# Kernel optimization log

Measured on AMD Instinct MI355X. Metric: run time of the kernel, lower is better.

Reference implementation:

```python
import jax, jax.numpy as jnp
import numpy as np

V, E, B, C = 10000, 128, 16, 128
N_REL = 8

def setup_inputs() -> dict:
    key = jax.random.key(0)
    k1, k2, k3, k4, k5 = jax.random.split(key, 5)
    src = jax.random.randint(k1, (B, C), 0, V, dtype=jnp.int32)
    src_embed = jax.random.normal(k2, (B, C, E), dtype=jnp.float32)
    embed_weight = jax.random.normal(k3, (V, E), dtype=jnp.float32)
    edge_matrix = jax.random.uniform(k4, (V, V), dtype=jnp.float32)
    relation_matrix = jax.random.randint(k5, (V, V), 0, 9, dtype=jnp.int32)
    return {"src": src, "src_embed": src_embed, "embed_weight": embed_weight,
            "edge_matrix": edge_matrix, "relation_matrix": relation_matrix}

def reference(src, src_embed, embed_weight, edge_matrix, relation_matrix):
    # base scores against full vocab: [B, C, V]
    base = jnp.einsum('bce,ve->bcv', src_embed, embed_weight)
    # gather the rows of both tables once: [B, C, V]
    edge_rows = edge_matrix[src]
    rel_rows = relation_matrix[src]
    concept_embeddings = []
    scores = []
    for i in range(N_REL):
        # ((relation_matrix == i+1) * edge_matrix)[src] > 0, gathered form
        mask = (jnp.where(rel_rows == i + 1, edge_rows, 0.0) > 0).astype(base.dtype)
        concept_weights = mask * base                     # [B, C, V]
        attn = jax.nn.softmax(concept_weights, axis=2)     # softmax over full vocab
        ce = jnp.einsum('bcv,ve->bce', attn, embed_weight) # [B, C, E]
        concept_embeddings.append(ce)
        scores.append(jnp.sum(src_embed * ce, axis=2, keepdims=True))
    scores = jnp.concatenate(scores, axis=2)               # [B, C, 8]
    weights = jax.nn.softmax(scores, axis=2)
    final = jnp.zeros_like(src_embed)
    for i in range(N_REL):
        final = final + weights[:, :, i:i + 1] * concept_embeddings[i]
    return final
```

## Files before the change

### kernel.cpp

```cpp
#include <hip/hip_runtime.h>

#define VV 10000
#define EE 128
#define NROWS 2048
#define NSPLIT 16

__global__ __launch_bounds__(256) void k1_base_gemm(
    const float* __restrict__ SE,
    const float* __restrict__ W,
    float* __restrict__ base)
{
    __shared__ float As[32 * 132];
    __shared__ float Ws[32 * 132];
    const int tid = threadIdx.x;
    const int v0 = blockIdx.x * 128;
    const int n0 = blockIdx.y * 128;
    const int tx = tid & 15;
    const int ty = tid >> 4;

    float acc[8][8];
    #pragma unroll
    for (int i = 0; i < 8; i++)
        #pragma unroll
        for (int j = 0; j < 8; j++) acc[i][j] = 0.f;

    for (int e0 = 0; e0 < EE; e0 += 32) {
        #pragma unroll
        for (int p = 0; p < 4; p++) {
            int f = tid + p * 256;
            int row = f >> 3;
            int c4  = f & 7;
            float4 a = *(const float4*)(SE + (n0 + row) * EE + e0 + c4 * 4);
            As[(c4 * 4 + 0) * 132 + row] = a.x;
            As[(c4 * 4 + 1) * 132 + row] = a.y;
            As[(c4 * 4 + 2) * 132 + row] = a.z;
            As[(c4 * 4 + 3) * 132 + row] = a.w;
            int vrow = v0 + row;
            float4 b = (vrow < VV) ? *(const float4*)(W + vrow * EE + e0 + c4 * 4)
                                   : make_float4(0.f, 0.f, 0.f, 0.f);
            Ws[(c4 * 4 + 0) * 132 + row] = b.x;
            Ws[(c4 * 4 + 1) * 132 + row] = b.y;
            Ws[(c4 * 4 + 2) * 132 + row] = b.z;
            Ws[(c4 * 4 + 3) * 132 + row] = b.w;
        }
        __syncthreads();
        #pragma unroll 4
        for (int kk = 0; kk < 32; kk++) {
            float4 a0 = *(const float4*)(As + kk * 132 + ty * 8);
            float4 a1 = *(const float4*)(As + kk * 132 + ty * 8 + 4);
            float4 b0 = *(const float4*)(Ws + kk * 132 + tx * 8);
            float4 b1 = *(const float4*)(Ws + kk * 132 + tx * 8 + 4);
            float av[8] = {a0.x, a0.y, a0.z, a0.w, a1.x, a1.y, a1.z, a1.w};
            float bv[8] = {b0.x, b0.y, b0.z, b0.w, b1.x, b1.y, b1.z, b1.w};
            #pragma unroll
            for (int i = 0; i < 8; i++)
                #pragma unroll
                for (int j = 0; j < 8; j++)
                    acc[i][j] = fmaf(av[i], bv[j], acc[i][j]);
        }
        __syncthreads();
    }

    #pragma unroll
    for (int i = 0; i < 8; i++) {
        int n = n0 + ty * 8 + i;
        float* brow = base + (long long)n * VV;
        #pragma unroll
        for (int jj = 0; jj < 2; jj++) {
            int v = v0 + tx * 8 + jj * 4;
            if (v < VV)
                *(float4*)(brow + v) = make_float4(acc[i][jj * 4 + 0], acc[i][jj * 4 + 1],
                                                   acc[i][jj * 4 + 2], acc[i][jj * 4 + 3]);
        }
    }
}

__global__ __launch_bounds__(256) void k2_stats(
    const int*   __restrict__ src,
    const float* __restrict__ edge,
    const int*   __restrict__ rel,
    float* __restrict__ baseA)
{
    __shared__ float seb[VV];
    __shared__ unsigned char srb[VV];
    __shared__ float wred[33][4];
    __shared__ float fin[33];
    __shared__ float cvals[12];

    const int n = blockIdx.x;
    const int tid = threadIdx.x;
    const int lane = tid & 63;
    const int wv = tid >> 6;
    const int s = src[n];
    const float4* brow4 = (const float4*)(baseA + (long long)n * VV);
    const float4* erow4 = (const float4*)(edge + (long long)s * VV);
    const int4*   rrow4 = (const int4*)(rel + (long long)s * VV);

    float accv[33];
    #pragma unroll
    for (int i = 0; i < 33; i++) accv[i] = 0.f;

    for (int v4 = tid; v4 < VV / 4; v4 += 256) {
        float4 b = brow4[v4];
        float4 e = erow4[v4];
        int4   r = rrow4[v4];
        float bb[4] = {b.x, b.y, b.z, b.w};
        float ee[4] = {e.x, e.y, e.z, e.w};
        int   rr[4] = {r.x, r.y, r.z, r.w};
        #pragma unroll
        for (int c = 0; c < 4; c++) {
            int rb = (rr[c] >= 1 && rr[c] <= 8 && ee[c] > 0.f) ? rr[c] : 0;
            float bc = bb[c];
            float eb = __expf(bc);
            float beb = bc * eb;
            seb[v4 * 4 + c] = eb;
            srb[v4 * 4 + c] = (unsigned char)rb;
            accv[0] += bc;
            #pragma unroll
            for (int q = 0; q < 8; q++) {
                float m = (rb == q + 1) ? 1.f : 0.f;
                accv[1 + q]  += m;
                accv[9 + q]  = fmaf(m, bc,  accv[9 + q]);
                accv[17 + q] = fmaf(m, eb,  accv[17 + q]);
                accv[25 + q] = fmaf(m, beb, accv[25 + q]);
            }
        }
    }

    #pragma unroll
    for (int i = 0; i < 33; i++) {
        float x = accv[i];
        #pragma unroll
        for (int off = 32; off > 0; off >>= 1) x += __shfl_xor(x, off, 64);
        if (lane == 0) wred[i][wv] = x;
    }
    __syncthreads();
    if (tid < 33)
        fin[tid] = wred[tid][0] + wred[tid][1] + wred[tid][2] + wred[tid][3];
    __syncthreads();

    if (tid == 0) {
        float sumbase = fin[0];
        float sc[8], Z[8];
        float smax = -1e30f;
        #pragma unroll
        for (int q = 0; q < 8; q++) {
            Z[q]  = ((float)VV - fin[1 + q]) + fin[17 + q];
            sc[q] = (sumbase - fin[9 + q] + fin[25 + q]) / Z[q];
            smax = fmaxf(smax, sc[q]);
        }
        float wsum = 0.f, wq[8];
        #pragma unroll
        for (int q = 0; q < 8; q++) { wq[q] = __expf(sc[q] - smax); wsum += wq[q]; }
        float Kc = 0.f;
        #pragma unroll
        for (int q = 0; q < 8; q++) {
            float c = (wq[q] / wsum) / Z[q];
            cvals[1 + q] = c;
            Kc += c;
        }
        cvals[0] = 0.f;
        cvals[9] = Kc;
    }
    __syncthreads();

    const float Kc = cvals[9];
    float4* broww = (float4*)(baseA + (long long)n * VV);
    for (int v4 = tid; v4 < VV / 4; v4 += 256) {
        float o[4];
        #pragma unroll
        for (int c = 0; c < 4; c++) {
            float eb = seb[v4 * 4 + c];
            float cc = cvals[srb[v4 * 4 + c]];
            o[c] = fmaf(cc, eb - 1.f, Kc);
        }
        broww[v4] = make_float4(o[0], o[1], o[2], o[3]);
    }
}

__global__ __launch_bounds__(256) void k3_gemm(
    const float* __restrict__ A,
    const float* __restrict__ W,
    float* __restrict__ part)
{
    __shared__ float As[32 * 68];
    __shared__ float Ws[32 * 132];
    const int tid = threadIdx.x;
    const int m0 = blockIdx.x * 64;
    const int ks = blockIdx.y;
    const int tx = tid & 15;
    const int ty = tid >> 4;

    float acc[4][8];
    #pragma unroll
    for (int i = 0; i < 4; i++)
        #pragma unroll
        for (int j = 0; j < 8; j++) acc[i][j] = 0.f;

    for (int kt = ks; kt < 313; kt += NSPLIT) {
        int k0 = kt * 32;
        #pragma unroll
        for (int p = 0; p < 2; p++) {
            int f = tid + p * 256;
            int row = f >> 3;
            int c4  = f & 7;
            int k = k0 + c4 * 4;
            float4 a = (k < VV) ? *(const float4*)(A + (long long)(m0 + row) * VV + k)
                                : make_float4(0.f, 0.f, 0.f, 0.f);
            As[(c4 * 4 + 0) * 68 + row] = a.x;
            As[(c4 * 4 + 1) * 68 + row] = a.y;
            As[(c4 * 4 + 2) * 68 + row] = a.z;
            As[(c4 * 4 + 3) * 68 + row] = a.w;
        }
        #pragma unroll
        for (int p = 0; p < 4; p++) {
            int f = tid + p * 256;
            int krow = f >> 5;
            int c4   = f & 31;
            int k = k0 + krow;
            float4 w4 = (k < VV) ? *(const float4*)(W + (long long)k * EE + c4 * 4)
                                 : make_float4(0.f, 0.f, 0.f, 0.f);
            *(float4*)(Ws + krow * 132 + c4 * 4) = w4;
        }
        __syncthreads();
        #pragma unroll 4
        for (int kk = 0; kk < 32; kk++) {
            float4 a4 = *(const float4*)(As + kk * 68 + ty * 4);
            float4 b0 = *(const float4*)(Ws + kk * 132 + tx * 8);
            float4 b1 = *(const float4*)(Ws + kk * 132 + tx * 8 + 4);
            float av[4] = {a4.x, a4.y, a4.z, a4.w};
            float bv[8] = {b0.x, b0.y, b0.z, b0.w, b1.x, b1.y, b1.z, b1.w};
            #pragma unroll
            for (int i = 0; i < 4; i++)
                #pragma unroll
                for (int j = 0; j < 8; j++)
                    acc[i][j] = fmaf(av[i], bv[j], acc[i][j]);
        }
        __syncthreads();
    }

    float* pp = part + (long long)ks * NROWS * EE;
    #pragma unroll
    for (int i = 0; i < 4; i++) {
        int m = m0 + ty * 4 + i;
        *(float4*)(pp + m * EE + tx * 8)     = make_float4(acc[i][0], acc[i][1], acc[i][2], acc[i][3]);
        *(float4*)(pp + m * EE + tx * 8 + 4) = make_float4(acc[i][4], acc[i][5], acc[i][6], acc[i][7]);
    }
}

__global__ __launch_bounds__(256) void k4_reduce(
    const float* __restrict__ part, float* __restrict__ out)
{
    int idx = blockIdx.x * 256 + threadIdx.x;
    const float4* p = (const float4*)part;
    const int stride = NROWS * EE / 4;
    float4 s = p[idx];
    #pragma unroll
    for (int k = 1; k < NSPLIT; k++) {
        float4 t = p[idx + k * stride];
        s.x += t.x; s.y += t.y; s.z += t.z; s.w += t.w;
    }
    ((float4*)out)[idx] = s;
}

extern "C" void kernel_launch(void* const* d_in, const int* in_sizes, int n_in,
                              void* d_out, int out_size, void* d_ws, size_t ws_size,
                              hipStream_t stream) {
    const int*   src  = (const int*)  d_in[0];
    const float* SE   = (const float*)d_in[1];
    const float* W    = (const float*)d_in[2];
    const float* edge = (const float*)d_in[3];
    const int*   rel  = (const int*)  d_in[4];
    float* out  = (float*)d_out;
    float* base = (float*)d_ws;
    float* part = base + (long long)NROWS * VV;

    k1_base_gemm<<<dim3(79, 16), 256, 0, stream>>>(SE, W, base);
    k2_stats<<<dim3(NROWS), 256, 0, stream>>>(src, edge, rel, base);
    k3_gemm<<<dim3(32, NSPLIT), 256, 0, stream>>>(base, W, part);
    k4_reduce<<<dim3(256), 256, 0, stream>>>(part, out);
}
```

Baseline: 806.4 us.

## Replace FP32 SIMT GEMMs with split-bf16 MFMA GEMMs and prepacked operands

Adds a prep kernel that splits SE and W, plus a transposed copy of W, into high and low bf16 halves stored in MFMA fragment layout. Both GEMMs (base scores and attention times W) then run as three bf16 MFMA products (hi*hi, hi*lo, lo*hi) to approximate fp32 accuracy on matrix cores instead of FP32 FMAs through LDS. The second GEMM converts A to split bf16 on the fly and doubles the split-K factor to 32. The cost is an extra launch, extra workspace, larger partial-sum reduction traffic, uncoalesced scalar output stores, and slightly reduced precision.

After: 738.5 us. -8.4%, faster.

```diff
diff --git a/kernel.cpp b/kernel.cpp
--- a/kernel.cpp
+++ b/kernel.cpp
@@ -3,74 +3,138 @@
 #define VV 10000
 #define EE 128
 #define NROWS 2048
-#define NSPLIT 16
-
-__global__ __launch_bounds__(256) void k1_base_gemm(
+#define KS 32
+
+typedef unsigned short u16;
+using short8 = __attribute__((ext_vector_type(8))) short;
+using f32x4  = __attribute__((ext_vector_type(4))) float;
+
+__device__ __forceinline__ u16 f2bf(float x) {
+    unsigned u = __float_as_uint(x);
+    return (u16)((u + 0x7fffu + ((u >> 16) & 1u)) >> 16);
+}
+__device__ __forceinline__ float bf2f(u16 h) {
+    return __uint_as_float(((unsigned)h) << 16);
+}
+
+__global__ __launch_bounds__(256) void k0_prep(
     const float* __restrict__ SE,
     const float* __restrict__ W,
+    u16* __restrict__ SEh, u16* __restrict__ SEl,
+    u16* __restrict__ Wh,  u16* __restrict__ Wl,
+    u16* __restrict__ WTh, u16* __restrict__ WTl)
+{
+    const int u = blockIdx.x * 256 + threadIdx.x;
+    float x[8];
+    u16 *dh, *dl;
+
+    if (u < 32768) {
+        int fid = u >> 6, l = u & 63;
+        int nf = fid >> 2, kt = fid & 3;
+        int row = nf * 16 + (l & 15);
+        int k0 = kt * 32 + (l >> 4) * 8;
+        const float* p = SE + row * EE + k0;
+        float4 a = *(const float4*)p, b = *(const float4*)(p + 4);
+        x[0]=a.x; x[1]=a.y; x[2]=a.z; x[3]=a.w;
+        x[4]=b.x; x[5]=b.y; x[6]=b.z; x[7]=b.w;
+        dh = SEh + u * 8; dl = SEl + u * 8;
+    } else if (u < 192768) {
+        int u2 = u - 32768;
+        int fid = u2 >> 6, l = u2 & 63;
+        int vf = fid >> 2, kt = fid & 3;
+        int row = vf * 16 + (l & 15);
+        int k0 = kt * 32 + (l >> 4) * 8;
+        const float* p = W + row * EE + k0;
+        float4 a = *(const float4*)p, b = *(const float4*)(p + 4);
+        x[0]=a.x; x[1]=a.y; x[2]=a.z; x[3]=a.w;
+        x[4]=b.x; x[5]=b.y; x[6]=b.z; x[7]=b.w;
+        dh = Wh + u2 * 8; dl = Wl + u2 * 8;
+    } else {
+        int u3 = u - 192768;
+        int fid = u3 >> 6, l = u3 & 63;
+        int ef = fid / 313, kc = fid - ef * 313;
+        int e  = ef * 16 + (l & 15);
+        int k8 = kc * 32 + (l >> 4) * 8;
+        if (k8 < VV) {
+            #pragma unroll
+            for (int i = 0; i < 8; i++) x[i] = W[(k8 + i) * EE + e];
+        } else {
+            #pragma unroll
+            for (int i = 0; i < 8; i++) x[i] = 0.f;
+        }
+        dh = WTh + u3 * 8; dl = WTl + u3 * 8;
+    }
+
+    short8 hv, lv;
+    #pragma unroll
+    for (int i = 0; i < 8; i++) {
+        u16 hb = f2bf(x[i]);
+        hv[i] = (short)hb;
+        lv[i] = (short)f2bf(x[i] - bf2f(hb));
+    }
+    *(short8*)dh = hv;
+    *(short8*)dl = lv;
+}
+
+__global__ __launch_bounds__(256) void k1_mfma(
+    const u16* __restrict__ SEh, const u16* __restrict__ SEl,
+    const u16* __restrict__ Wh,  const u16* __restrict__ Wl,
     float* __restrict__ base)
 {
-    __shared__ float As[32 * 132];
-    __shared__ float Ws[32 * 132];
     const int tid = threadIdx.x;
-    const int v0 = blockIdx.x * 128;
-    const int n0 = blockIdx.y * 128;
-    const int tx = tid & 15;
-    const int ty = tid >> 4;
-
-    float acc[8][8];
-    #pragma unroll
-    for (int i = 0; i < 8; i++)
-        #pragma unroll
-        for (int j = 0; j < 8; j++) acc[i][j] = 0.f;
-
-    for (int e0 = 0; e0 < EE; e0 += 32) {
-        #pragma unroll
-        for (int p = 0; p < 4; p++) {
-            int f = tid + p * 256;
-            int row = f >> 3;
-            int c4  = f & 7;
-            float4 a = *(const float4*)(SE + (n0 + row) * EE + e0 + c4 * 4);
-            As[(c4 * 4 + 0) * 132 + row] = a.x;
-            As[(c4 * 4 + 1) * 132 + row] = a.y;
-            As[(c4 * 4 + 2) * 132 + row] = a.z;
-            As[(c4 * 4 + 3) * 132 + row] = a.w;
-            int vrow = v0 + row;
-            float4 b = (vrow < VV) ? *(const float4*)(W + vrow * EE + e0 + c4 * 4)
-                                   : make_float4(0.f, 0.f, 0.f, 0.f);
-            Ws[(c4 * 4 + 0) * 132 + row] = b.x;
-            Ws[(c4 * 4 + 1) * 132 + row] = b.y;
-            Ws[(c4 * 4 + 2) * 132 + row] = b.z;
-            Ws[(c4 * 4 + 3) * 132 + row] = b.w;
-        }
-        __syncthreads();
-        #pragma unroll 4
-        for (int kk = 0; kk < 32; kk++) {
-            float4 a0 = *(const float4*)(As + kk * 132 + ty * 8);
-            float4 a1 = *(const float4*)(As + kk * 132 + ty * 8 + 4);
-            float4 b0 = *(const float4*)(Ws + kk * 132 + tx * 8);
-            float4 b1 = *(const float4*)(Ws + kk * 132 + tx * 8 + 4);
-            float av[8] = {a0.x, a0.y, a0.z, a0.w, a1.x, a1.y, a1.z, a1.w};
-            float bv[8] = {b0.x, b0.y, b0.z, b0.w, b1.x, b1.y, b1.z, b1.w};
-            #pragma unroll
-            for (int i = 0; i < 8; i++)
-                #pragma unroll
-                for (int j = 0; j < 8; j++)
-                    acc[i][j] = fmaf(av[i], bv[j], acc[i][j]);
-        }
-        __syncthreads();
-    }
-
-    #pragma unroll
-    for (int i = 0; i < 8; i++) {
-        int n = n0 + ty * 8 + i;
-        float* brow = base + (long long)n * VV;
-        #pragma unroll
-        for (int jj = 0; jj < 2; jj++) {
-            int v = v0 + tx * 8 + jj * 4;
-            if (v < VV)
-                *(float4*)(brow + v) = make_float4(acc[i][jj * 4 + 0], acc[i][jj * 4 + 1],
-                                                   acc[i][jj * 4 + 2], acc[i][jj * 4 + 3]);
+    const int l = tid & 63, wv = tid >> 6;
+    const int wn = wv >> 1, wq = wv & 1;
+    const int vt = blockIdx.x, nt = blockIdx.y;
+    const int nf0 = nt * 4 + wn * 2;
+    const int vf0 = vt * 8 + wq * 4;
+
+    f32x4 acc[2][4];
+    #pragma unroll
+    for (int i = 0; i < 2; i++)
+        #pragma unroll
+        for (int j = 0; j < 4; j++)
+            acc[i][j] = (f32x4){0.f, 0.f, 0.f, 0.f};
+
+    #pragma unroll
+    for (int kt = 0; kt < 4; ++kt) {
+        short8 ah[2], al[2];
+        #pragma unroll
+        for (int i = 0; i < 2; ++i) {
+            int off = (((nf0 + i) * 4 + kt) * 64 + l) * 8;
+            ah[i] = *(const short8*)(SEh + off);
+            al[i] = *(const short8*)(SEl + off);
+        }
+        #pragma unroll
+        for (int j = 0; j < 4; ++j) {
+            int vf = vf0 + j;
+            short8 bh = {0,0,0,0,0,0,0,0};
+            short8 bl = {0,0,0,0,0,0,0,0};
+            if (vf < 625) {
+                int off = ((vf * 4 + kt) * 64 + l) * 8;
+                bh = *(const short8*)(Wh + off);
+                bl = *(const short8*)(Wl + off);
+            }
+            #pragma unroll
+            for (int i = 0; i < 2; ++i) {
+                acc[i][j] = __builtin_amdgcn_mfma_f32_16x16x32_bf16(ah[i], bh, acc[i][j], 0, 0, 0);
+                acc[i][j] = __builtin_amdgcn_mfma_f32_16x16x32_bf16(ah[i], bl, acc[i][j], 0, 0, 0);
+                acc[i][j] = __builtin_amdgcn_mfma_f32_16x16x32_bf16(al[i], bh, acc[i][j], 0, 0, 0);
+            }
+        }
+    }
+
+    const int c = l & 15, r0 = (l >> 4) * 4;
+    #pragma unroll
+    for (int j = 0; j < 4; ++j) {
+        int vf = vf0 + j;
+        if (vf >= 625) continue;
+        int v = vf * 16 + c;
+        #pragma unroll
+        for (int i = 0; i < 2; ++i) {
+            int n = (nf0 + i) * 16 + r0;
+            #pragma unroll
+            for (int r = 0; r < 4; ++r)
+                base[(n + r) * VV + v] = acc[i][j][r];
         }
     }
 }
@@ -178,73 +242,72 @@
     }
 }
 
-__global__ __launch_bounds__(256) void k3_gemm(
+__global__ __launch_bounds__(256) void k3_mfma(
     const float* __restrict__ A,
-    const float* __restrict__ W,
+    const u16* __restrict__ WTh, const u16* __restrict__ WTl,
     float* __restrict__ part)
 {
-    __shared__ float As[32 * 68];
-    __shared__ float Ws[32 * 132];
     const int tid = threadIdx.x;
-    const int m0 = blockIdx.x * 64;
-    const int ks = blockIdx.y;
-    const int tx = tid & 15;
-    const int ty = tid >> 4;
-
-    float acc[4][8];
-    #pragma unroll
-    for (int i = 0; i < 4; i++)
-        #pragma unroll
-        for (int j = 0; j < 8; j++) acc[i][j] = 0.f;
-
-    for (int kt = ks; kt < 313; kt += NSPLIT) {
-        int k0 = kt * 32;
-        #pragma unroll
-        for (int p = 0; p < 2; p++) {
-            int f = tid + p * 256;
-            int row = f >> 3;
-            int c4  = f & 7;
-            int k = k0 + c4 * 4;
-            float4 a = (k < VV) ? *(const float4*)(A + (long long)(m0 + row) * VV + k)
-                                : make_float4(0.f, 0.f, 0.f, 0.f);
-            As[(c4 * 4 + 0) * 68 + row] = a.x;
-            As[(c4 * 4 + 1) * 68 + row] = a.y;
-            As[(c4 * 4 + 2) * 68 + row] = a.z;
-            As[(c4 * 4 + 3) * 68 + row] = a.w;
-        }
-        #pragma unroll
-        for (int p = 0; p < 4; p++) {
-            int f = tid + p * 256;
-            int krow = f >> 5;
-            int c4   = f & 31;
-            int k = k0 + krow;
-            float4 w4 = (k < VV) ? *(const float4*)(W + (long long)k * EE + c4 * 4)
-                                 : make_float4(0.f, 0.f, 0.f, 0.f);
-            *(float4*)(Ws + krow * 132 + c4 * 4) = w4;
-        }
-        __syncthreads();
-        #pragma unroll 4
-        for (int kk = 0; kk < 32; kk++) {
-            float4 a4 = *(const float4*)(As + kk * 68 + ty * 4);
-            float4 b0 = *(const float4*)(Ws + kk * 132 + tx * 8);
-            float4 b1 = *(const float4*)(Ws + kk * 132 + tx * 8 + 4);
-            float av[4] = {a4.x, a4.y, a4.z, a4.w};
-            float bv[8] = {b0.x, b0.y, b0.z, b0.w, b1.x, b1.y, b1.z, b1.w};
-            #pragma unroll
-            for (int i = 0; i < 4; i++)
+    const int l = tid & 63, wv = tid >> 6;
+    const int mt = blockIdx.x, ks = blockIdx.y;
+    const int mf0 = mt * 8 + wv * 2;
+    const int g = l >> 4, rr_ = l & 15;
+
+    f32x4 acc[2][8];
+    #pragma unroll
+    for (int i = 0; i < 2; i++)
+        #pragma unroll
+        for (int j = 0; j < 8; j++)
+            acc[i][j] = (f32x4){0.f, 0.f, 0.f, 0.f};
+
+    for (int kc = ks; kc < 313; kc += KS) {
+        int k8 = kc * 32 + g * 8;
+        short8 ah[2], al[2];
+        #pragma unroll
+        for (int i = 0; i < 2; ++i) {
+            float x[8];
+            if (k8 < VV) {
+                const float* p = A + ((mf0 + i) * 16 + rr_) * VV + k8;
+                float4 a = *(const float4*)p, b = *(const float4*)(p + 4);
+                x[0]=a.x; x[1]=a.y; x[2]=a.z; x[3]=a.w;
+                x[4]=b.x; x[5]=b.y; x[6]=b.z; x[7]=b.w;
+            } else {
                 #pragma unroll
-                for (int j = 0; j < 8; j++)
-                    acc[i][j] = fmaf(av[i], bv[j], acc[i][j]);
-        }
-        __syncthreads();
+                for (int q = 0; q < 8; q++) x[q] = 0.f;
+            }
+            #pragma unroll
+            for (int q = 0; q < 8; q++) {
+                u16 hb = f2bf(x[q]);
+                ah[i][q] = (short)hb;
+                al[i][q] = (short)f2bf(x[q] - bf2f(hb));
+            }
+        }
+        #pragma unroll
+        for (int j = 0; j < 8; ++j) {
+            int off = ((j * 313 + kc) * 64 + l) * 8;
+            short8 bh = *(const short8*)(WTh + off);
+            short8 bl = *(const short8*)(WTl + off);
+            #pragma unroll
+            for (int i = 0; i < 2; ++i) {
+                acc[i][j] = __builtin_amdgcn_mfma_f32_16x16x32_bf16(ah[i], bh, acc[i][j], 0, 0, 0);
+                acc[i][j] = __builtin_amdgcn_mfma_f32_16x16x32_bf16(ah[i], bl, acc[i][j], 0, 0, 0);
+                acc[i][j] = __builtin_amdgcn_mfma_f32_16x16x32_bf16(al[i], bh, acc[i][j], 0, 0, 0);
+            }
+        }
     }
 
     float* pp = part + (long long)ks * NROWS * EE;
-    #pragma unroll
-    for (int i = 0; i < 4; i++) {
-        int m = m0 + ty * 4 + i;
-        *(float4*)(pp + m * EE + tx * 8)     = make_float4(acc[i][0], acc[i][1], acc[i][2], acc[i][3]);
-        *(float4*)(pp + m * EE + tx * 8 + 4) = make_float4(acc[i][4], acc[i][5], acc[i][6], acc[i][7]);
+    const int c = l & 15, r0 = g * 4;
+    #pragma unroll
+    for (int i = 0; i < 2; ++i) {
+        #pragma unroll
+        for (int j = 0; j < 8; ++j) {
+            int e = j * 16 + c;
+            int m = (mf0 + i) * 16 + r0;
+            #pragma unroll
+            for (int r = 0; r < 4; ++r)
+                pp[(m + r) * EE + e] = acc[i][j][r];
+        }
     }
 }
 
@@ -256,7 +319,7 @@
     const int stride = NROWS * EE / 4;
     float4 s = p[idx];
     #pragma unroll
-    for (int k = 1; k < NSPLIT; k++) {
+    for (int k = 1; k < KS; k++) {
         float4 t = p[idx + k * stride];
         s.x += t.x; s.y += t.y; s.z += t.z; s.w += t.w;
     }
@@ -272,11 +335,19 @@
     const float* edge = (const float*)d_in[3];
     const int*   rel  = (const int*)  d_in[4];
     float* out  = (float*)d_out;
+
     float* base = (float*)d_ws;
     float* part = base + (long long)NROWS * VV;
-
-    k1_base_gemm<<<dim3(79, 16), 256, 0, stream>>>(SE, W, base);
+    u16* SEh = (u16*)(part + (long long)KS * NROWS * EE);
+    u16* SEl = SEh + 262144;
+    u16* Wh  = SEl + 262144;
+    u16* Wl  = Wh  + 1280000;
+    u16* WTh = Wl  + 1280000;
+    u16* WTl = WTh + 1282048;
+
+    k0_prep<<<dim3(1379), 256, 0, stream>>>(SE, W, SEh, SEl, Wh, Wl, WTh, WTl);
+    k1_mfma<<<dim3(79, 32), 256, 0, stream>>>(SEh, SEl, Wh, Wl, base);
     k2_stats<<<dim3(NROWS), 256, 0, stream>>>(src, edge, rel, base);
-    k3_gemm<<<dim3(32, NSPLIT), 256, 0, stream>>>(base, W, part);
+    k3_mfma<<<dim3(16, KS), 256, 0, stream>>>(base, WTh, WTl, part);
     k4_reduce<<<dim3(256), 256, 0, stream>>>(part, out);
 }
```
